# Kernel tuning notes

Hardware: AMD Instinct MI355X
Metric: run time of the kernel (lower is better)

The kernel has to match this reference:

```python
import jax, jax.numpy as jnp
import numpy as np

B, C, Ci, H, W = 8, 256, 128, 64, 64
EPS = 1e-5


def conv1x1(x, w, b):
    # x: [B,C,H,W], w: [O,C], b: [O] -> [B,O,H,W]
    return jnp.einsum('bchw,oc->bohw', x, w) + b[None, :, None, None]


def maxpool2(x):
    b, c, h, w = x.shape
    return x.reshape(b, c, h // 2, 2, w // 2, 2).max(axis=(3, 5))


def setup_inputs() -> dict:
    key = jax.random.key(0)
    ks = jax.random.split(key, 12)
    s_in = 1.0 / np.sqrt(C)
    s_ic = 1.0 / np.sqrt(Ci)
    return {
        'x': jax.random.normal(ks[0], (B, C, H, W), dtype=jnp.float32),
        'g_w': jax.random.normal(ks[1], (Ci, C), dtype=jnp.float32) * s_in,
        'g_b': jax.random.normal(ks[2], (Ci,), dtype=jnp.float32) * 0.01,
        'theta_w': jax.random.normal(ks[3], (Ci, C), dtype=jnp.float32) * s_in,
        'theta_b': jax.random.normal(ks[4], (Ci,), dtype=jnp.float32) * 0.01,
        'phi_w': jax.random.normal(ks[5], (Ci, C), dtype=jnp.float32) * s_in,
        'phi_b': jax.random.normal(ks[6], (Ci,), dtype=jnp.float32) * 0.01,
        'W_w': jax.random.normal(ks[7], (C, Ci), dtype=jnp.float32) * s_ic,
        'W_b': jax.random.normal(ks[8], (C,), dtype=jnp.float32) * 0.01,
        'bn_gamma': jax.random.normal(ks[9], (C,), dtype=jnp.float32) * 0.1 + 1.0,
        'bn_beta': jax.random.normal(ks[10], (C,), dtype=jnp.float32) * 0.1,
        'bn_mean': jnp.zeros((C,), dtype=jnp.float32),
        'bn_var': jax.random.uniform(ks[11], (C,), dtype=jnp.float32) * 0.5 + 0.75,
    }


def reference(x, g_w, g_b, theta_w, theta_b, phi_w, phi_b, W_w, W_b, bn_gamma, bn_beta, bn_mean, bn_var):
    b = x.shape[0]
    # g and phi: 1x1 conv then 2x2 max-pool (sub_sample=True)
    g_x = maxpool2(conv1x1(x, g_w, g_b)).reshape(b, Ci, -1)          # [B,Ci,Np]
    g_x = jnp.transpose(g_x, (0, 2, 1))                               # [B,Np,Ci]
    theta_x = conv1x1(x, theta_w, theta_b).reshape(b, Ci, -1)         # [B,Ci,N]
    theta_x = jnp.transpose(theta_x, (0, 2, 1))                       # [B,N,Ci]
    phi_x = maxpool2(conv1x1(x, phi_w, phi_b)).reshape(b, Ci, -1)     # [B,Ci,Np]
    f = jnp.einsum('bnc,bcm->bnm', theta_x, phi_x)                    # [B,N,Np]
    f_div_C = jax.nn.softmax(f, axis=-1)                              # embedded_gaussian: plain softmax, no scaling
    y = jnp.einsum('bnm,bmc->bnc', f_div_C, g_x)                      # [B,N,Ci]
    y = jnp.transpose(y, (0, 2, 1)).reshape(b, Ci, H, W)              # [B,Ci,H,W]
    # W: 1x1 conv + BatchNorm (inference form with running stats)
    W_y = conv1x1(y, W_w, W_b)
    inv = bn_gamma / jnp.sqrt(bn_var + EPS)
    W_y = (W_y - bn_mean[None, :, None, None]) * inv[None, :, None, None] + bn_beta[None, :, None, None]
    return W_y + x
```

## Files before the change

kernel.cpp:

```cpp
#include <hip/hip_runtime.h>
#include <math.h>

#define Bn   8
#define Cc   256
#define Cin  128
#define Hh   64
#define Ww   64
#define Nn   4096
#define Npl  1024
#define EPSf 1e-5f

typedef __attribute__((ext_vector_type(8))) short    short8;
typedef __attribute__((ext_vector_type(8))) _Float16 half8;
typedef __attribute__((ext_vector_type(4))) float    floatx4;

__device__ __forceinline__ unsigned short f2bf(float f) {
    unsigned int u = __float_as_uint(f);
    u += 0x7fffu + ((u >> 16) & 1u);
    return (unsigned short)(u >> 16);
}
__device__ __forceinline__ unsigned short f2h(float f) {
    _Float16 h = (_Float16)f;
    return __builtin_bit_cast(unsigned short, h);
}
__device__ __forceinline__ float h2f(unsigned short u) {
    return (float)__builtin_bit_cast(_Float16, u);
}

__device__ __forceinline__ unsigned int cvtpk_bf16(float lo, float hi) {
    unsigned int r;
    asm("v_cvt_pk_bf16_f32 %0, %1, %2" : "=v"(r) : "v"(lo), "v"(hi));
    return r;
}

__device__ __forceinline__ void gload_lds16(const unsigned short* g, unsigned short* l) {
    __builtin_amdgcn_global_load_lds(
        (const __attribute__((address_space(1))) unsigned int*)g,
        (__attribute__((address_space(3))) unsigned int*)l, 16, 0, 0);
}

__global__ __launch_bounds__(256) void k_prep(
    const float* __restrict__ g_w, const float* __restrict__ th_w,
    const float* __restrict__ ph_w,
    const float* __restrict__ W_w, const float* __restrict__ W_b,
    const float* __restrict__ gamma, const float* __restrict__ beta,
    const float* __restrict__ mean,  const float* __restrict__ var,
    unsigned short* __restrict__ gWh,
    unsigned short* __restrict__ thWh, unsigned short* __restrict__ thWl,
    unsigned short* __restrict__ phWh, unsigned short* __restrict__ phWl,
    unsigned short* __restrict__ Wh, float* __restrict__ cvec)
{
    int i = blockIdx.x * 256 + threadIdx.x;
    if (i < 98304) {
        int seg = i >> 15;
        int idx = i & 32767;
        int o = idx >> 8;
        int c = idx & 255;
        int p = (((o >> 4) * 8 + (c >> 5)) * 64
                 + ((c >> 3) & 3) * 16 + (o & 15)) * 8 + (c & 7);
        float v = (seg == 0 ? g_w : (seg == 1 ? th_w : ph_w))[idx];
        unsigned short hi = f2h(v);
        if (seg == 0) gWh[p] = hi;
        else {
            (seg == 1 ? thWh : phWh)[p] = hi;
            (seg == 1 ? thWl : phWl)[p] = f2h(v - h2f(hi));
        }
    } else {
        int j = i - 98304;
        int o = j >> 7;
        float inv = gamma[o] * rsqrtf(var[o] + EPSf);
        Wh[j] = f2h(W_w[j] * inv);
        if (j < Cc) {
            float invi = gamma[j] * rsqrtf(var[j] + EPSf);
            cvec[j] = (W_b[j] - mean[j]) * invi + beta[j];
        }
    }
}

#define XPAD 264

__global__ __launch_bounds__(256, 2) void k_conv3(
    const float* __restrict__ x,
    const unsigned short* __restrict__ gWh,
    const unsigned short* __restrict__ thWh, const unsigned short* __restrict__ thWl,
    const unsigned short* __restrict__ phWh, const unsigned short* __restrict__ phWl,
    const float* __restrict__ g_b, const float* __restrict__ th_b,
    const float* __restrict__ ph_b,
    unsigned short* __restrict__ thetaT,
    unsigned short* __restrict__ gPc,
    unsigned short* __restrict__ phiPt)
{
    __shared__ __align__(16) unsigned short Xhi[64 * XPAD];
    __shared__ __align__(16) unsigned short Xlo[64 * XPAD];

    const int t    = threadIdx.x;
    const int w    = t >> 6;
    const int l    = t & 63;
    const int quad = l >> 4;
    const int l16  = l & 15;
    const int b    = blockIdx.x >> 6;
    const int tile = blockIdx.x & 63;
    const int ty   = tile >> 1;
    const int tx   = tile & 1;

    {
        const float4* xg = (const float4*)x;
        unsigned int* XhiW = (unsigned int*)Xhi;
        unsigned int* XloW = (unsigned int*)Xlo;
        #pragma unroll
        for (int it = 0; it < 8; ++it) {
            int idx = t + 256 * it;
            int c2  = idx >> 4;
            int p4  = idx & 15;
            int n   = (2 * ty + (p4 >> 3)) * Ww + tx * 32 + (p4 & 7) * 4;
            float4 va = xg[((size_t)(b * Cc + 2 * c2) * Nn + n) >> 2];
            float4 vb = xg[((size_t)(b * Cc + 2 * c2 + 1) * Nn + n) >> 2];
            const float fa[4] = {va.x, va.y, va.z, va.w};
            const float fb[4] = {vb.x, vb.y, vb.z, vb.w};
            #pragma unroll
            for (int i = 0; i < 4; ++i) {
                int px = p4 * 4 + i;
                unsigned short ha = f2h(fa[i]), hb = f2h(fb[i]);
                unsigned short la = f2h(fa[i] - h2f(ha));
                unsigned short lb = f2h(fb[i] - h2f(hb));
                XhiW[px * 132 + c2] = (unsigned int)ha | ((unsigned int)hb << 16);
                XloW[px * 132 + c2] = (unsigned int)la | ((unsigned int)lb << 16);
            }
        }
    }
    __syncthreads();

    floatx4 acc[6][4] = {};

    #pragma unroll 2
    for (int kd = 0; kd < 8; ++kd) {
        half8 bhi[4], blo[4];
        #pragma unroll
        for (int nt = 0; nt < 4; ++nt) {
            bhi[nt] = *(const half8*)&Xhi[(nt * 16 + l16) * XPAD + kd * 32 + quad * 8];
            blo[nt] = *(const half8*)&Xlo[(nt * 16 + l16) * XPAD + kd * 32 + quad * 8];
        }
        #pragma unroll
        for (int ti = 0; ti < 6; ++ti) {
            int ot  = w + 4 * ti;
            int seg = ot >> 3;
            size_t aoff = (size_t)(((ot & 7) * 8 + kd) * 512 + l * 8);
            const unsigned short* wh = (seg == 0 ? gWh : (seg == 1 ? thWh : phWh));
            half8 ah = *(const half8*)&wh[aoff];
            #pragma unroll
            for (int nt = 0; nt < 4; ++nt)
                acc[ti][nt] = __builtin_amdgcn_mfma_f32_16x16x32_f16(ah, bhi[nt], acc[ti][nt], 0, 0, 0);
            if (seg != 0) {
                const unsigned short* wl = (seg == 1 ? thWl : phWl);
                half8 al = *(const half8*)&wl[aoff];
                #pragma unroll
                for (int nt = 0; nt < 4; ++nt) {
                    acc[ti][nt] = __builtin_amdgcn_mfma_f32_16x16x32_f16(ah, blo[nt], acc[ti][nt], 0, 0, 0);
                    acc[ti][nt] = __builtin_amdgcn_mfma_f32_16x16x32_f16(al, bhi[nt], acc[ti][nt], 0, 0, 0);
                }
            }
        }
    }

    #pragma unroll
    for (int ti = 0; ti < 6; ++ti) {
        int ot  = w + 4 * ti;
        int seg = ot >> 3;
        int ol  = (ot & 7) * 16 + quad * 4;
        if (seg == 1) {
            float b0 = th_b[ol], b1 = th_b[ol + 1], b2 = th_b[ol + 2], b3 = th_b[ol + 3];
            #pragma unroll
            for (int nt = 0; nt < 4; ++nt) {
                int n = (2 * ty + (nt >> 1)) * Ww + tx * 32 + (nt & 1) * 16 + l16;
                ushort4 v;
                v.x = f2h(acc[ti][nt][0] + b0);
                v.y = f2h(acc[ti][nt][1] + b1);
                v.z = f2h(acc[ti][nt][2] + b2);
                v.w = f2h(acc[ti][nt][3] + b3);
                *(ushort4*)&thetaT[((size_t)b * Nn + n) * Cin + ol] = v;
            }
        } else {
            const float* bb = (seg == 0 ? g_b : ph_b);
            float b0 = bb[ol], b1 = bb[ol + 1], b2 = bb[ol + 2], b3 = bb[ol + 3];
            #pragma unroll
            for (int pp = 0; pp < 2; ++pp) {
                float pm[4];
                #pragma unroll
                for (int r = 0; r < 4; ++r) {
                    float m = fmaxf(acc[ti][pp][r], acc[ti][pp + 2][r]);
                    pm[r] = fmaxf(m, __shfl_xor(m, 1, 64));
                }
                int np = ty * 32 + tx * 16 + pp * 8 + (l16 >> 1);
                if ((l16 & 1) == 0) {
                    if (seg == 0) {
                        gPc[((size_t)b * Cin + ol + 0) * Npl + np] = f2bf(pm[0] + b0);
                        gPc[((size_t)b * Cin + ol + 1) * Npl + np] = f2bf(pm[1] + b1);
                        gPc[((size_t)b * Cin + ol + 2) * Npl + np] = f2bf(pm[2] + b2);
                        gPc[((size_t)b * Cin + ol + 3) * Npl + np] = f2bf(pm[3] + b3);
                    } else {
                        ushort4 v;
                        v.x = f2h(pm[0] + b0); v.y = f2h(pm[1] + b1);
                        v.z = f2h(pm[2] + b2); v.w = f2h(pm[3] + b3);
                        *(ushort4*)&phiPt[((size_t)b * Npl + np) * Cin + ol] = v;
                    }
                }
            }
        }
    }
}

__device__ __forceinline__ void stage_kv(
    unsigned short* smem, int sel, int chg, int b, int grp, int wq,
    int mK, int gK, int cV, int gV,
    const unsigned short* __restrict__ phiPt,
    const unsigned short* __restrict__ gPc)
{
    unsigned short* Kb = smem + sel * 16384;
    if (grp == 0) {
        #pragma unroll
        for (int j = 0; j < 4; ++j) {
            int slot = wq * 4 + j;
            int m  = slot * 4 + mK;
            int gs = gK ^ (m & 7);
            gload_lds16(&phiPt[((size_t)b * Npl + chg * 64 + m) * Cin + gs * 8],
                        &Kb[slot * 512]);
        }
    } else {
        unsigned short* Vb = Kb + 8192;
        #pragma unroll
        for (int j = 0; j < 4; ++j) {
            int slot = wq * 4 + j;
            int c  = slot * 8 + cV;
            int gs = gV ^ (c & 7);
            gload_lds16(&gPc[((size_t)b * Cin + c) * Npl + chg * 64 + gs * 8],
                        &Vb[slot * 512]);
        }
    }
}

#define SSHIFT 20.0f

__global__ __launch_bounds__(512, 2) void k_attn_out(
    const unsigned short* __restrict__ thetaT,
    const unsigned short* __restrict__ phiPt,
    const unsigned short* __restrict__ gPc,
    const unsigned short* __restrict__ Wh,
    const float* __restrict__ cvec,
    const float* __restrict__ x,
    float* __restrict__ out)
{
    __shared__ __align__(16) unsigned short smem[65536];

    const int t    = threadIdx.x;
    const int w    = t >> 6;
    const int wq   = w & 3;
    const int grp  = w >> 2;
    const int l    = t & 63;
    const int quad = l >> 4;
    const int l16  = l & 15;
    const int bid  = blockIdx.x;
    const int wid  = (bid & 7) * 64 + (bid >> 3);
    const int b    = wid >> 6;
    const int qb   = wid & 63;
    const int n0   = qb * 64;

    uint4 qr[4];
    #pragma unroll
    for (int kd = 0; kd < 4; ++kd)
        qr[kd] = *(const uint4*)&thetaT[((size_t)b * Nn + n0 + wq * 16 + l16) * Cin
                                        + kd * 32 + quad * 8];
    #pragma unroll
    for (int kd = 0; kd < 4; ++kd)
        asm volatile("" : "+v"(qr[kd].x), "+v"(qr[kd].y), "+v"(qr[kd].z), "+v"(qr[kd].w));
    half8 qf[4];
    #pragma unroll
    for (int kd = 0; kd < 4; ++kd) qf[kd] = __builtin_bit_cast(half8, qr[kd]);

    floatx4 yacc[8] = {};
    float liq = 0.f;

    const int mK = l >> 4;
    const int gK = l & 15;
    const int cV = l >> 3;
    const int gV = l & 7;

    #pragma unroll
    for (int pc = 0; pc < 3; ++pc)
        stage_kv(smem, pc, pc, b, grp, wq, mK, gK, cV, gV, phiPt, gPc);
    asm volatile("s_waitcnt vmcnt(8)" ::: "memory");
    __builtin_amdgcn_s_barrier();

    for (int ch = 0; ch < 16; ++ch) {
        if (ch < 13)
            stage_kv(smem, (ch + 3) & 3, ch + 3, b, grp, wq, mK, gK, cV, gV, phiPt, gPc);

        const unsigned short* Ks = smem + (ch & 3) * 16384;
        const unsigned short* Vt = Ks + 8192;

        floatx4 sacc[2] = {};
        #pragma unroll
        for (int mtl = 0; mtl < 2; ++mtl) {
            int mt = grp * 2 + mtl;
            #pragma unroll
            for (int kd = 0; kd < 4; ++kd) {
                half8 kf = *(const half8*)&Ks[(mt * 16 + l16) * 128
                                              + (((kd * 4 + quad) ^ (l16 & 7)) << 3)];
                sacc[mtl] = __builtin_amdgcn_mfma_f32_16x16x32_f16(kf, qf[kd], sacc[mtl], 0, 0, 0);
            }
        }

        float ex0[4], ex1[4];
        #pragma unroll
        for (int r = 0; r < 4; ++r) {
            ex0[r] = __expf(sacc[0][r] - SSHIFT);
            ex1[r] = __expf(sacc[1][r] - SSHIFT);
            liq += ex0[r] + ex1[r];
        }

        unsigned int a0 = cvtpk_bf16(ex0[0], ex0[1]);
        unsigned int a1 = cvtpk_bf16(ex1[0], ex1[1]);
        unsigned int b0 = cvtpk_bf16(ex0[2], ex0[3]);
        unsigned int b1 = cvtpk_bf16(ex1[2], ex1[3]);
        asm volatile("v_permlane32_swap_b32 %0, %1" : "+v"(a0), "+v"(a1));
        asm volatile("v_permlane16_swap_b32 %0, %1" : "+v"(a0), "+v"(a1));
        asm volatile("v_permlane32_swap_b32 %0, %1" : "+v"(b0), "+v"(b1));
        asm volatile("v_permlane16_swap_b32 %0, %1" : "+v"(b0), "+v"(b1));
        uint4 pw; pw.x = a0; pw.y = b0; pw.z = a1; pw.w = b1;
        short8 pf = __builtin_bit_cast(short8, pw);

        #pragma unroll
        for (int ct = 0; ct < 8; ++ct) {
            short8 vf = *(const short8*)&Vt[(ct * 16 + l16) * 64
                                            + (((grp * 4 + quad) ^ (l16 & 7)) << 3)];
            yacc[ct] = __builtin_amdgcn_mfma_f32_16x16x32_bf16(pf, vf, yacc[ct], 0, 0, 0);
        }

        if (ch < 13)       asm volatile("s_waitcnt vmcnt(8)" ::: "memory");
        else if (ch == 13) asm volatile("s_waitcnt vmcnt(4)" ::: "memory");
        else if (ch == 14) asm volatile("s_waitcnt vmcnt(0)" ::: "memory");
        __builtin_amdgcn_s_barrier();
    }

    liq += __shfl_xor(liq, 16, 64);
    liq += __shfl_xor(liq, 32, 64);

    float* cbuf = (float*)smem;
    const int ci = (wq * 64 + l) * 33;
    if (grp == 1) {
        #pragma unroll
        for (int ct = 0; ct < 8; ++ct)
            #pragma unroll
            for (int r = 0; r < 4; ++r) cbuf[ci + ct * 4 + r] = yacc[ct][r];
        cbuf[ci + 32] = liq;
    }
    __syncthreads();
    if (grp == 0) {
        #pragma unroll
        for (int ct = 0; ct < 8; ++ct)
            #pragma unroll
            for (int r = 0; r < 4; ++r) yacc[ct][r] += cbuf[ci + ct * 4 + r];
        liq += cbuf[ci + 32];
    }
    __syncthreads();

    {
        unsigned short* Ws = smem + 8192;
        #pragma unroll
        for (int j = 0; j < 8; ++j) {
            int slot = w * 8 + j;
            int row  = slot * 4 + mK;
            int gs   = gK ^ (row & 7);
            gload_lds16(&Wh[(size_t)row * Cin + gs * 8], &Ws[slot * 512]);
        }
    }

    if (grp == 0) {
        unsigned int* Yw = (unsigned int*)smem;
        #pragma unroll
        for (int r = 0; r < 4; ++r) {
            float lr = __shfl(liq, quad * 4 + r, 64);
            float il = 1.0f / lr;
            int q  = wq * 16 + quad * 4 + r;
            int q7 = q & 7;
            #pragma unroll
            for (int ct = 0; ct < 8; ++ct) {
                unsigned int h = f2h(yacc[ct][r] * il);
                unsigned int p = (unsigned int)__shfl_xor((int)h, 1, 64);
                if ((l16 & 1) == 0) {
                    int g = ct * 2 + (l16 >> 3);
                    Yw[q * 64 + (((g ^ q7) << 2) | ((l16 & 7) >> 1))] = h | (p << 16);
                }
            }
        }
    }
    asm volatile("s_waitcnt vmcnt(0)" ::: "memory");
    __syncthreads();

    const unsigned short* Ys = smem;
    const unsigned short* Ws = smem + 8192;

    half8 af[2][4];
    #pragma unroll
    for (int mt = 0; mt < 2; ++mt)
        #pragma unroll
        for (int kd = 0; kd < 4; ++kd) {
            int row = w * 32 + mt * 16 + l16;
            af[mt][kd] = *(const half8*)&Ws[row * 128
                                            + (((kd * 4 + quad) ^ (l16 & 7)) << 3)];
        }

    floatx4 acc[2][4] = {};
    #pragma unroll
    for (int nt = 0; nt < 4; ++nt) {
        half8 bfr[4];
        #pragma unroll
        for (int kd = 0; kd < 4; ++kd)
            bfr[kd] = *(const half8*)&Ys[(nt * 16 + l16) * 128
                                         + (((kd * 4 + quad) ^ (l16 & 7)) << 3)];
        #pragma unroll
        for (int mt = 0; mt < 2; ++mt)
            #pragma unroll
            for (int kd = 0; kd < 4; ++kd)
                acc[mt][nt] = __builtin_amdgcn_mfma_f32_16x16x32_f16(af[mt][kd], bfr[kd], acc[mt][nt], 0, 0, 0);
    }

    #pragma unroll
    for (int mt = 0; mt < 2; ++mt) {
        #pragma unroll
        for (int r = 0; r < 4; ++r) {
            int o = w * 32 + mt * 16 + quad * 4 + r;
            float cv = cvec[o];
            #pragma unroll
            for (int nt = 0; nt < 4; ++nt) {
                size_t gi = ((size_t)(b * Cc + o)) * Nn + n0 + nt * 16 + l16;
                out[gi] = acc[mt][nt][r] + cv + x[gi];
            }
        }
    }
}

extern "C" void kernel_launch(void* const* d_in, const int* in_sizes, int n_in,
                              void* d_out, int out_size, void* d_ws, size_t ws_size,
                              hipStream_t stream) {
    const float* x    = (const float*)d_in[0];
    const float* g_w  = (const float*)d_in[1];
    const float* g_b  = (const float*)d_in[2];
    const float* th_w = (const float*)d_in[3];
    const float* th_b = (const float*)d_in[4];
    const float* ph_w = (const float*)d_in[5];
    const float* ph_b = (const float*)d_in[6];
    const float* W_w  = (const float*)d_in[7];
    const float* W_b  = (const float*)d_in[8];
    const float* gmm  = (const float*)d_in[9];
    const float* bta  = (const float*)d_in[10];
    const float* mmn  = (const float*)d_in[11];
    const float* vvr  = (const float*)d_in[12];
    float* out = (float*)d_out;

    unsigned short* thetaT = (unsigned short*)d_ws;
    unsigned short* phiPt  = thetaT + (size_t)4194304;
    unsigned short* gPc    = phiPt + (size_t)1048576;
    unsigned short* Wh     = gPc + (size_t)1048576;
    unsigned short* gWh    = Wh + 32768;
    unsigned short* thWh   = gWh + 32768;
    unsigned short* thWl   = thWh + 32768;
    unsigned short* phWh   = thWl + 32768;
    unsigned short* phWl   = phWh + 32768;
    float*          cvec   = (float*)(phWl + 32768);

    k_prep<<<dim3(512), dim3(256), 0, stream>>>(
        g_w, th_w, ph_w, W_w, W_b, gmm, bta, mmn, vvr,
        gWh, thWh, thWl, phWh, phWl, Wh, cvec);
    k_conv3<<<dim3(Bn * 64), dim3(256), 0, stream>>>(
        x, gWh, thWh, thWl, phWh, phWl, g_b, th_b, ph_b, thetaT, gPc, phiPt);
    k_attn_out<<<dim3(Bn * 64), dim3(512), 0, stream>>>(
        thetaT, phiPt, gPc, Wh, cvec, x, out);
}
```

Measured before the change: 180.5 us.

## Double query tile per attention block and widen conv kernel to 512 threads

The attention kernel now processes 128 queries per block instead of 64, with each wave holding two query fragments, so every staged K/V chunk in shared memory feeds twice the MFMA work. The grid is halved to 256 blocks. The conv kernel moves to 512 threads, with each wave computing one output tile per segment, giving more waves per block. The goal is to cut K/V load and staging traffic per query. The cost is doubled accumulator registers and fewer blocks, which can lower occupancy and leave CUs under-filled.

```diff
diff --git a/kernel.cpp b/kernel.cpp
--- a/kernel.cpp
+++ b/kernel.cpp
@@ -79,7 +79,7 @@
 
 #define XPAD 264
 
-__global__ __launch_bounds__(256, 2) void k_conv3(
+__global__ __launch_bounds__(512, 4) void k_conv3(
     const float* __restrict__ x,
     const unsigned short* __restrict__ gWh,
     const unsigned short* __restrict__ thWh, const unsigned short* __restrict__ thWl,
@@ -108,8 +108,8 @@
         unsigned int* XhiW = (unsigned int*)Xhi;
         unsigned int* XloW = (unsigned int*)Xlo;
         #pragma unroll
-        for (int it = 0; it < 8; ++it) {
-            int idx = t + 256 * it;
+        for (int it = 0; it < 4; ++it) {
+            int idx = t + 512 * it;
             int c2  = idx >> 4;
             int p4  = idx & 15;
             int n   = (2 * ty + (p4 >> 3)) * Ww + tx * 32 + (p4 & 7) * 4;
@@ -130,7 +130,7 @@
     }
     __syncthreads();
 
-    floatx4 acc[6][4] = {};
+    floatx4 acc[3][4] = {};
 
     #pragma unroll 2
     for (int kd = 0; kd < 8; ++kd) {
@@ -141,10 +141,9 @@
             blo[nt] = *(const half8*)&Xlo[(nt * 16 + l16) * XPAD + kd * 32 + quad * 8];
         }
         #pragma unroll
-        for (int ti = 0; ti < 6; ++ti) {
-            int ot  = w + 4 * ti;
-            int seg = ot >> 3;
-            size_t aoff = (size_t)(((ot & 7) * 8 + kd) * 512 + l * 8);
+        for (int ti = 0; ti < 3; ++ti) {
+            int seg = ti;
+            size_t aoff = (size_t)((w * 8 + kd) * 512 + l * 8);
             const unsigned short* wh = (seg == 0 ? gWh : (seg == 1 ? thWh : phWh));
             half8 ah = *(const half8*)&wh[aoff];
             #pragma unroll
@@ -163,10 +162,9 @@
     }
 
     #pragma unroll
-    for (int ti = 0; ti < 6; ++ti) {
-        int ot  = w + 4 * ti;
-        int seg = ot >> 3;
-        int ol  = (ot & 7) * 16 + quad * 4;
+    for (int ti = 0; ti < 3; ++ti) {
+        int seg = ti;
+        int ol  = w * 16 + quad * 4;
         if (seg == 1) {
             float b0 = th_b[ol], b1 = th_b[ol + 1], b2 = th_b[ol + 2], b3 = th_b[ol + 3];
             #pragma unroll
@@ -259,25 +257,33 @@
     const int quad = l >> 4;
     const int l16  = l & 15;
     const int bid  = blockIdx.x;
-    const int wid  = (bid & 7) * 64 + (bid >> 3);
-    const int b    = wid >> 6;
-    const int qb   = wid & 63;
-    const int n0   = qb * 64;
-
-    uint4 qr[4];
-    #pragma unroll
-    for (int kd = 0; kd < 4; ++kd)
-        qr[kd] = *(const uint4*)&thetaT[((size_t)b * Nn + n0 + wq * 16 + l16) * Cin
-                                        + kd * 32 + quad * 8];
-    #pragma unroll
-    for (int kd = 0; kd < 4; ++kd)
-        asm volatile("" : "+v"(qr[kd].x), "+v"(qr[kd].y), "+v"(qr[kd].z), "+v"(qr[kd].w));
-    half8 qf[4];
-    #pragma unroll
-    for (int kd = 0; kd < 4; ++kd) qf[kd] = __builtin_bit_cast(half8, qr[kd]);
-
-    floatx4 yacc[8] = {};
-    float liq = 0.f;
+    const int wid  = (bid & 7) * 32 + (bid >> 3);
+    const int b    = wid >> 5;
+    const int qb   = wid & 31;
+    const int n0   = qb * 128;
+
+    uint4 qr0[4], qr1[4];
+    #pragma unroll
+    for (int kd = 0; kd < 4; ++kd) {
+        qr0[kd] = *(const uint4*)&thetaT[((size_t)b * Nn + n0 + wq * 32 + l16) * Cin
+                                         + kd * 32 + quad * 8];
+        qr1[kd] = *(const uint4*)&thetaT[((size_t)b * Nn + n0 + wq * 32 + 16 + l16) * Cin
+                                         + kd * 32 + quad * 8];
+    }
+    #pragma unroll
+    for (int kd = 0; kd < 4; ++kd) {
+        asm volatile("" : "+v"(qr0[kd].x), "+v"(qr0[kd].y), "+v"(qr0[kd].z), "+v"(qr0[kd].w));
+        asm volatile("" : "+v"(qr1[kd].x), "+v"(qr1[kd].y), "+v"(qr1[kd].z), "+v"(qr1[kd].w));
+    }
+    half8 qf0[4], qf1[4];
+    #pragma unroll
+    for (int kd = 0; kd < 4; ++kd) {
+        qf0[kd] = __builtin_bit_cast(half8, qr0[kd]);
+        qf1[kd] = __builtin_bit_cast(half8, qr1[kd]);
+    }
+
+    floatx4 yacc0[8] = {}, yacc1[8] = {};
+    float liq0 = 0.f, liq1 = 0.f;
 
     const int mK = l >> 4;
     const int gK = l & 15;
@@ -297,7 +303,7 @@
         const unsigned short* Ks = smem + (ch & 3) * 16384;
         const unsigned short* Vt = Ks + 8192;
 
-        floatx4 sacc[2] = {};
+        floatx4 sacc0[2] = {}, sacc1[2] = {};
         #pragma unroll
         for (int mtl = 0; mtl < 2; ++mtl) {
             int mt = grp * 2 + mtl;
@@ -305,34 +311,57 @@
             for (int kd = 0; kd < 4; ++kd) {
                 half8 kf = *(const half8*)&Ks[(mt * 16 + l16) * 128
                                               + (((kd * 4 + quad) ^ (l16 & 7)) << 3)];
-                sacc[mtl] = __builtin_amdgcn_mfma_f32_16x16x32_f16(kf, qf[kd], sacc[mtl], 0, 0, 0);
-            }
-        }
-
-        float ex0[4], ex1[4];
-        #pragma unroll
-        for (int r = 0; r < 4; ++r) {
-            ex0[r] = __expf(sacc[0][r] - SSHIFT);
-            ex1[r] = __expf(sacc[1][r] - SSHIFT);
-            liq += ex0[r] + ex1[r];
-        }
-
-        unsigned int a0 = cvtpk_bf16(ex0[0], ex0[1]);
-        unsigned int a1 = cvtpk_bf16(ex1[0], ex1[1]);
-        unsigned int b0 = cvtpk_bf16(ex0[2], ex0[3]);
-        unsigned int b1 = cvtpk_bf16(ex1[2], ex1[3]);
-        asm volatile("v_permlane32_swap_b32 %0, %1" : "+v"(a0), "+v"(a1));
-        asm volatile("v_permlane16_swap_b32 %0, %1" : "+v"(a0), "+v"(a1));
-        asm volatile("v_permlane32_swap_b32 %0, %1" : "+v"(b0), "+v"(b1));
-        asm volatile("v_permlane16_swap_b32 %0, %1" : "+v"(b0), "+v"(b1));
-        uint4 pw; pw.x = a0; pw.y = b0; pw.z = a1; pw.w = b1;
-        short8 pf = __builtin_bit_cast(short8, pw);
+                sacc0[mtl] = __builtin_amdgcn_mfma_f32_16x16x32_f16(kf, qf0[kd], sacc0[mtl], 0, 0, 0);
+                sacc1[mtl] = __builtin_amdgcn_mfma_f32_16x16x32_f16(kf, qf1[kd], sacc1[mtl], 0, 0, 0);
+            }
+        }
+
+        short8 pf0, pf1;
+        {
+            float e0[4], e1[4];
+            #pragma unroll
+            for (int r = 0; r < 4; ++r) {
+                e0[r] = __expf(sacc0[0][r] - SSHIFT);
+                e1[r] = __expf(sacc0[1][r] - SSHIFT);
+                liq0 += e0[r] + e1[r];
+            }
+            unsigned int a0 = cvtpk_bf16(e0[0], e0[1]);
+            unsigned int a1 = cvtpk_bf16(e1[0], e1[1]);
+            unsigned int b0 = cvtpk_bf16(e0[2], e0[3]);
+            unsigned int b1 = cvtpk_bf16(e1[2], e1[3]);
+            asm volatile("v_permlane32_swap_b32 %0, %1" : "+v"(a0), "+v"(a1));
+            asm volatile("v_permlane16_swap_b32 %0, %1" : "+v"(a0), "+v"(a1));
+            asm volatile("v_permlane32_swap_b32 %0, %1" : "+v"(b0), "+v"(b1));
+            asm volatile("v_permlane16_swap_b32 %0, %1" : "+v"(b0), "+v"(b1));
+            uint4 pw; pw.x = a0; pw.y = b0; pw.z = a1; pw.w = b1;
+            pf0 = __builtin_bit_cast(short8, pw);
+        }
+        {
+            float e0[4], e1[4];
+            #pragma unroll
+            for (int r = 0; r < 4; ++r) {
+                e0[r] = __expf(sacc1[0][r] - SSHIFT);
+                e1[r] = __expf(sacc1[1][r] - SSHIFT);
+                liq1 += e0[r] + e1[r];
+            }
+            unsigned int a0 = cvtpk_bf16(e0[0], e0[1]);
+            unsigned int a1 = cvtpk_bf16(e1[0], e1[1]);
+            unsigned int b0 = cvtpk_bf16(e0[2], e0[3]);
+            unsigned int b1 = cvtpk_bf16(e1[2], e1[3]);
+            asm volatile("v_permlane32_swap_b32 %0, %1" : "+v"(a0), "+v"(a1));
+            asm volatile("v_permlane16_swap_b32 %0, %1" : "+v"(a0), "+v"(a1));
+            asm volatile("v_permlane32_swap_b32 %0, %1" : "+v"(b0), "+v"(b1));
+            asm volatile("v_permlane16_swap_b32 %0, %1" : "+v"(b0), "+v"(b1));
+            uint4 pw; pw.x = a0; pw.y = b0; pw.z = a1; pw.w = b1;
+            pf1 = __builtin_bit_cast(short8, pw);
+        }
 
         #pragma unroll
         for (int ct = 0; ct < 8; ++ct) {
             short8 vf = *(const short8*)&Vt[(ct * 16 + l16) * 64
                                             + (((grp * 4 + quad) ^ (l16 & 7)) << 3)];
-            yacc[ct] = __builtin_amdgcn_mfma_f32_16x16x32_bf16(pf, vf, yacc[ct], 0, 0, 0);
+            yacc0[ct] = __builtin_amdgcn_mfma_f32_16x16x32_bf16(pf0, vf, yacc0[ct], 0, 0, 0);
+            yacc1[ct] = __builtin_amdgcn_mfma_f32_16x16x32_bf16(pf1, vf, yacc1[ct], 0, 0, 0);
         }
 
         if (ch < 13)       asm volatile("s_waitcnt vmcnt(8)" ::: "memory");
@@ -341,30 +370,41 @@
         __builtin_amdgcn_s_barrier();
     }
 
-    liq += __shfl_xor(liq, 16, 64);
-    liq += __shfl_xor(liq, 32, 64);
+    liq0 += __shfl_xor(liq0, 16, 64);
+    liq0 += __shfl_xor(liq0, 32, 64);
+    liq1 += __shfl_xor(liq1, 16, 64);
+    liq1 += __shfl_xor(liq1, 32, 64);
 
     float* cbuf = (float*)smem;
-    const int ci = (wq * 64 + l) * 33;
+    const int ci0 = ((wq * 2 + 0) * 64 + l) * 33;
+    const int ci1 = ((wq * 2 + 1) * 64 + l) * 33;
     if (grp == 1) {
         #pragma unroll
         for (int ct = 0; ct < 8; ++ct)
             #pragma unroll
-            for (int r = 0; r < 4; ++r) cbuf[ci + ct * 4 + r] = yacc[ct][r];
-        cbuf[ci + 32] = liq;
+            for (int r = 0; r < 4; ++r) {
+                cbuf[ci0 + ct * 4 + r] = yacc0[ct][r];
+                cbuf[ci1 + ct * 4 + r] = yacc1[ct][r];
+            }
+        cbuf[ci0 + 32] = liq0;
+        cbuf[ci1 + 32] = liq1;
     }
     __syncthreads();
     if (grp == 0) {
         #pragma unroll
         for (int ct = 0; ct < 8; ++ct)
             #pragma unroll
-            for (int r = 0; r < 4; ++r) yacc[ct][r] += cbuf[ci + ct * 4 + r];
-        liq += cbuf[ci + 32];
+            for (int r = 0; r < 4; ++r) {
+                yacc0[ct][r] += cbuf[ci0 + ct * 4 + r];
+                yacc1[ct][r] += cbuf[ci1 + ct * 4 + r];
+            }
+        liq0 += cbuf[ci0 + 32];
+        liq1 += cbuf[ci1 + 32];
     }
     __syncthreads();
 
     {
-        unsigned short* Ws = smem + 8192;
+        unsigned short* Ws = smem + 16384;
         #pragma unroll
         for (int j = 0; j < 8; ++j) {
             int slot = w * 8 + j;
@@ -378,17 +418,22 @@
         unsigned int* Yw = (unsigned int*)smem;
         #pragma unroll
         for (int r = 0; r < 4; ++r) {
-            float lr = __shfl(liq, quad * 4 + r, 64);
-            float il = 1.0f / lr;
-            int q  = wq * 16 + quad * 4 + r;
-            int q7 = q & 7;
+            float lr0 = __shfl(liq0, quad * 4 + r, 64);
+            float lr1 = __shfl(liq1, quad * 4 + r, 64);
+            float il0 = 1.0f / lr0;
+            float il1 = 1.0f / lr1;
+            int q0 = wq * 32 + quad * 4 + r;
+            int q1 = q0 + 16;
             #pragma unroll
             for (int ct = 0; ct < 8; ++ct) {
-                unsigned int h = f2h(yacc[ct][r] * il);
-                unsigned int p = (unsigned int)__shfl_xor((int)h, 1, 64);
+                unsigned int h0 = f2h(yacc0[ct][r] * il0);
+                unsigned int p0 = (unsigned int)__shfl_xor((int)h0, 1, 64);
+                unsigned int h1 = f2h(yacc1[ct][r] * il1);
+                unsigned int p1 = (unsigned int)__shfl_xor((int)h1, 1, 64);
                 if ((l16 & 1) == 0) {
                     int g = ct * 2 + (l16 >> 3);
-                    Yw[q * 64 + (((g ^ q7) << 2) | ((l16 & 7) >> 1))] = h | (p << 16);
+                    Yw[q0 * 64 + (((g ^ (q0 & 7)) << 2) | ((l16 & 7) >> 1))] = h0 | (p0 << 16);
+                    Yw[q1 * 64 + (((g ^ (q1 & 7)) << 2) | ((l16 & 7) >> 1))] = h1 | (p1 << 16);
                 }
             }
         }
@@ -397,7 +442,7 @@
     __syncthreads();
 
     const unsigned short* Ys = smem;
-    const unsigned short* Ws = smem + 8192;
+    const unsigned short* Ws = smem + 16384;
 
     half8 af[2][4];
     #pragma unroll
@@ -409,9 +454,9 @@
                                             + (((kd * 4 + quad) ^ (l16 & 7)) << 3)];
         }
 
-    floatx4 acc[2][4] = {};
-    #pragma unroll
-    for (int nt = 0; nt < 4; ++nt) {
+    floatx4 acc[2][8] = {};
+    #pragma unroll
+    for (int nt = 0; nt < 8; ++nt) {
         half8 bfr[4];
         #pragma unroll
         for (int kd = 0; kd < 4; ++kd)
@@ -431,7 +476,7 @@
             int o = w * 32 + mt * 16 + quad * 4 + r;
             float cv = cvec[o];
             #pragma unroll
-            for (int nt = 0; nt < 4; ++nt) {
+            for (int nt = 0; nt < 8; ++nt) {
                 size_t gi = ((size_t)(b * Cc + o)) * Nn + n0 + nt * 16 + l16;
                 out[gi] = acc[mt][nt][r] + cv + x[gi];
             }
@@ -471,8 +516,8 @@
     k_prep<<<dim3(512), dim3(256), 0, stream>>>(
         g_w, th_w, ph_w, W_w, W_b, gmm, bta, mmn, vvr,
         gWh, thWh, thWl, phWh, phWl, Wh, cvec);
-    k_conv3<<<dim3(Bn * 64), dim3(256), 0, stream>>>(
+    k_conv3<<<dim3(Bn * 64), dim3(512), 0, stream>>>(
         x, gWh, thWh, thWl, phWh, phWl, g_b, th_b, ph_b, thetaT, gPc, phiPt);
-    k_attn_out<<<dim3(Bn * 64), dim3(512), 0, stream>>>(
+    k_attn_out<<<dim3(Bn * 32), dim3(512), 0, stream>>>(
         thetaT, phiPt, gPc, Wh, cvec, x, out);
 }
```

New measurement: 156.9 us. 1.15x faster.
